# Kernel tuning notes

Measured on AMD Instinct MI355X. Metric: run time of the kernel, lower is better.

The kernel has to match this reference:

```python
import math
import jax, jax.numpy as jnp
import numpy as np

B = 512
E = 512
C = 70722
M_MARGIN = 0.4
H = 0.333
S = 64.0
T_ALPHA = 1.0
EPS = 1e-3


def setup_inputs() -> dict:
    key = jax.random.key(0)
    k1, k2, k3, k4 = jax.random.split(key, 4)
    embbedings = jax.random.normal(k1, (B, E), dtype=jnp.float32)
    embbedings = embbedings / jnp.linalg.norm(embbedings, axis=1, keepdims=True)
    # feature norms typically ~[10, 30] for face models
    norms = 10.0 + 20.0 * jax.random.uniform(k2, (B, 1), dtype=jnp.float32)
    label = jax.random.randint(k3, (B,), 0, C, dtype=jnp.int64)
    kernel = jax.random.normal(k4, (E, C), dtype=jnp.float32)
    batch_mean = jnp.ones((C,), dtype=jnp.float32) * 20.0
    batch_std = jnp.asarray(10.0, dtype=jnp.float32)
    return {"embbedings": embbedings, "norms": norms, "label": label,
            "kernel": kernel, "batch_mean": batch_mean, "batch_std": batch_std}


def reference(embbedings, norms, label, kernel, batch_mean, batch_std):
    # column-wise l2-normalize the class weight matrix [E, C]
    kernel_norm = kernel / jnp.linalg.norm(kernel, axis=0, keepdims=True)
    cosine = jnp.clip(embbedings @ kernel_norm, -1.0 + EPS, 1.0 - EPS)  # [B, C]
    safe_norms = jnp.clip(norms, 1e-3, 100.0)  # [B, 1]

    # ---- running-stat update (torch.no_grad block) ----
    sn = jax.lax.stop_gradient(safe_norms[:, 0])  # [B]
    sums = jnp.zeros((C,), dtype=sn.dtype).at[label].add(sn)
    counts = jnp.zeros((C,), dtype=sn.dtype).at[label].add(1.0)
    group_mean = sums / jnp.maximum(counts, 1.0)  # per-class batch mean of norms
    new_mean = jnp.where(counts > 0,
                         group_mean * T_ALPHA + (1.0 - T_ALPHA) * batch_mean,
                         batch_mean)
    std = jnp.std(sn, ddof=1)  # torch.std is unbiased
    new_std = std * T_ALPHA + (1.0 - T_ALPHA) * batch_std

    # ---- adaptive margin ----
    margin_scaler = (safe_norms - new_mean[label][:, None]) / (new_std + EPS)
    margin_scaler = jnp.clip(margin_scaler * H, -1.0, 1.0)  # [B, 1]

    oh = jax.nn.one_hot(label, C, dtype=cosine.dtype)  # [B, C]
    g_angular = -M_MARGIN * margin_scaler               # [B, 1]
    theta = jnp.arccos(cosine)
    theta_m = jnp.clip(theta + oh * g_angular, EPS, math.pi - EPS)
    g_add = M_MARGIN + M_MARGIN * margin_scaler         # [B, 1]
    out = (jnp.cos(theta_m) - oh * g_add) * S
    return out
```

## Files before the change

kernel.cpp:

```cpp
#include <hip/hip_runtime.h>
#include <hip/hip_bf16.h>
#include <cstdint>
#include <cstddef>
#include <math.h>

#define B_SZ 512
#define E_SZ 512
#define C_SZ 70722
#define PAD_C 70784
#define M_MARGIN 0.4f
#define H_CONST 0.333f
#define S_CONST 64.0f
#define EPS_F 1e-3f
#define PI_F 3.14159265358979323846f

typedef __attribute__((ext_vector_type(8))) short short8;
typedef __attribute__((ext_vector_type(4))) float f32x4;


__device__ __forceinline__ unsigned short f2bf(float x) {
  __hip_bfloat16 h = __float2bfloat16(x);
  unsigned short u;
  __builtin_memcpy(&u, &h, 2);
  return u;
}

__device__ __forceinline__ void gload_lds16(const void* g, void* l) {
  __builtin_amdgcn_global_load_lds(
      (const __attribute__((address_space(1))) unsigned int*)g,
      (__attribute__((address_space(3))) unsigned int*)l, 16, 0, 0);
}

__device__ __forceinline__ int swzb(int rc) {
  return (((rc & 7) ^ ((rc >> 2) & 7)) << 4);
}

__global__ void k_stats(const float* __restrict__ norms, const int* __restrict__ label,
                        float* __restrict__ ga, float* __restrict__ gadd) {
  __shared__ float sn[B_SZ];
  __shared__ int lab[B_SZ];
  __shared__ float redA[8], redB[8];
  __shared__ float sh_std;

  int t = threadIdx.x;
  float v = norms[t];
  v = fminf(fmaxf(v, 1e-3f), 100.0f);
  sn[t] = v;
  lab[t] = label[t];

  float s1 = v, s2 = v * v;
  #pragma unroll
  for (int o = 32; o > 0; o >>= 1) {
    s1 += __shfl_down(s1, o);
    s2 += __shfl_down(s2, o);
  }
  if ((t & 63) == 0) { redA[t >> 6] = s1; redB[t >> 6] = s2; }
  __syncthreads();
  if (t == 0) {
    float a = 0.f, b = 0.f;
    #pragma unroll
    for (int i = 0; i < 8; ++i) { a += redA[i]; b += redB[i]; }
    float mean = a / (float)B_SZ;
    float var = (b - (float)B_SZ * mean * mean) / (float)(B_SZ - 1);
    sh_std = sqrtf(fmaxf(var, 0.f));
  }
  __syncthreads();
  float stdv = sh_std;

  int myl = lab[t];
  float s = 0.f, cnt = 0.f;
  for (int j = 0; j < B_SZ; ++j) {
    bool m = (lab[j] == myl);
    s += m ? sn[j] : 0.f;
    cnt += m ? 1.f : 0.f;
  }
  float gm = s / fmaxf(cnt, 1.f);
  float ms = (v - gm) / (stdv + EPS_F) * H_CONST;
  ms = fminf(fmaxf(ms, -1.f), 1.f);
  ga[t] = -M_MARGIN * ms;
  gadd[t] = M_MARGIN + M_MARGIN * ms;
}

__global__ void k_cvtA(const float* __restrict__ emb, unsigned short* __restrict__ abf) {
  int i = (blockIdx.x * 256 + threadIdx.x) * 4;
  float4 f = *(const float4*)(emb + i);
  unsigned short u0 = f2bf(f.x), u1 = f2bf(f.y), u2 = f2bf(f.z), u3 = f2bf(f.w);
  unsigned long long pk = (unsigned long long)u0 | ((unsigned long long)u1 << 16) |
                          ((unsigned long long)u2 << 32) | ((unsigned long long)u3 << 48);
  *(unsigned long long*)(abf + i) = pk;
}

__global__ void k_colnorm(const float* __restrict__ K, float* __restrict__ inv) {
  __shared__ float part[4][64];
  int cl = threadIdx.x & 63;
  int rq = threadIdx.x >> 6;
  int c = blockIdx.x * 64 + cl;
  float s = 0.f;
  if (c < C_SZ) {
    const float* p = K + (size_t)rq * 128 * C_SZ + c;
    #pragma unroll 8
    for (int r = 0; r < 128; ++r) {
      float x = p[(size_t)r * C_SZ];
      s += x * x;
    }
  }
  part[rq][cl] = s;
  __syncthreads();
  if (threadIdx.x < 64) {
    int c2 = blockIdx.x * 64 + threadIdx.x;
    if (c2 < C_SZ) {
      float tt = part[0][threadIdx.x] + part[1][threadIdx.x] +
                 part[2][threadIdx.x] + part[3][threadIdx.x];
      inv[c2] = rsqrtf(tt);
    } else if (c2 < PAD_C) {
      inv[c2] = 0.f;
    }
  }
}

__launch_bounds__(256)
__global__ void k_gemm(const unsigned short* __restrict__ Abf,
                       const float* __restrict__ Kmat,
                       const float* __restrict__ invn,
                       const int* __restrict__ label,
                       const float* __restrict__ ga,
                       const float* __restrict__ gadd,
                       float* __restrict__ out) {
  __shared__ __align__(16) unsigned short As[128 * 64];
  __shared__ __align__(16) unsigned short Bs[128 * 64];
  __shared__ int lab_s[128];
  __shared__ float ga_s[128], gadd_s[128];

  const int tid = threadIdx.x;
  const int nwg = gridDim.x;
  int bid = blockIdx.x;

  int q = nwg >> 3, r8 = nwg & 7;
  int xcd = bid & 7, lb = bid >> 3;
  int wg = (xcd < r8 ? xcd * (q + 1) : r8 * (q + 1) + (xcd - r8) * q) + lb;

  const int mt = wg & 3;
  const int nt = wg >> 2;
  const int row0 = mt << 7;
  const int col0 = nt << 7;

  if (tid < 128) {
    int gr = row0 + tid;
    lab_s[tid] = label[gr];
    ga_s[tid] = ga[gr];
    gadd_s[tid] = gadd[gr];
  }

  const int wid = tid >> 6, lane = tid & 63;
  const int wr = wid >> 1, wc = wid & 1;

  const int cc = tid & 31;
  const int kq = tid >> 5;

  const bool edge = (col0 + 128 > C_SZ);
  float4 inv4 = *(const float4*)(invn + col0 + cc * 4);

  f32x4 acc[4][4];
  #pragma unroll
  for (int m = 0; m < 4; ++m)
    #pragma unroll
    for (int n = 0; n < 4; ++n)
      acc[m][n] = f32x4{0.f, 0.f, 0.f, 0.f};

  const float* Bg = Kmat + col0;

  for (int kt = 0; kt < 8; ++kt) {
    const int kb = kt * 64;
    if (kt) __syncthreads();

    #pragma unroll
    for (int rr = 0; rr < 4; ++rr) {
      int rowblk = wid * 32 + rr * 8;
      int r = rowblk + (lane >> 3);
      int s = (lane & 7) ^ ((r & 7) ^ ((r >> 2) & 7));
      const unsigned short* g = Abf + (size_t)(row0 + r) * 512 + kb + s * 8;
      gload_lds16(g, (char*)As + rowblk * 128);
    }

    #pragma unroll
    for (int i = 0; i < 4; ++i) {
      int k = (kq + i * 8) * 2;
      const float* g0 = Bg + (size_t)(kb + k) * C_SZ + cc * 4;
      const float* g1 = g0 + C_SZ;
      float x0[4], x1[4];
      if (!edge) {
        float4 f0 = *(const float4*)g0;
        float4 f1 = *(const float4*)g1;
        x0[0] = f0.x; x0[1] = f0.y; x0[2] = f0.z; x0[3] = f0.w;
        x1[0] = f1.x; x1[1] = f1.y; x1[2] = f1.z; x1[3] = f1.w;
      } else {
        #pragma unroll
        for (int j = 0; j < 4; ++j) {
          int gc = col0 + cc * 4 + j;
          x0[j] = (gc < C_SZ) ? g0[j] : 0.f;
          x1[j] = (gc < C_SZ) ? g1[j] : 0.f;
        }
      }
      #pragma unroll
      for (int j = 0; j < 4; ++j) {
        int c = cc * 4 + j;
        float iv = ((const float*)&inv4)[j];
        unsigned int pk = ((unsigned int)f2bf(x1[j] * iv) << 16) | (unsigned int)f2bf(x0[j] * iv);
        int byte = (c * 128 + k * 2) ^ swzb(c);
        *(unsigned int*)((char*)Bs + byte) = pk;
      }
    }

    __syncthreads();

    #pragma unroll
    for (int ks = 0; ks < 2; ++ks) {
      short8 a[4], b[4];
      #pragma unroll
      for (int m = 0; m < 4; ++m) {
        int row = wr * 64 + m * 16 + (lane & 15);
        int off = (row * 128 + ks * 64 + (lane >> 4) * 16) ^ swzb(row);
        a[m] = *(const short8*)((const char*)As + off);
      }
      #pragma unroll
      for (int n = 0; n < 4; ++n) {
        int c = wc * 64 + n * 16 + (lane & 15);
        int off = (c * 128 + ks * 64 + (lane >> 4) * 16) ^ swzb(c);
        b[n] = *(const short8*)((const char*)Bs + off);
      }
      #pragma unroll
      for (int m = 0; m < 4; ++m)
        #pragma unroll
        for (int n = 0; n < 4; ++n)
          acc[m][n] = __builtin_amdgcn_mfma_f32_16x16x32_bf16(a[m], b[n], acc[m][n], 0, 0, 0);
    }
  }

  #pragma unroll
  for (int m = 0; m < 4; ++m) {
    int rl0 = wr * 64 + m * 16 + ((lane >> 4) << 2);
    #pragma unroll
    for (int n = 0; n < 4; ++n) {
      int cl = wc * 64 + n * 16 + (lane & 15);
      int gc = col0 + cl;
      if (gc >= C_SZ) continue;
      #pragma unroll
      for (int r = 0; r < 4; ++r) {
        int rl = rl0 + r;
        float v = acc[m][n][r];
        v = fminf(fmaxf(v, -1.f + EPS_F), 1.f - EPS_F);
        float res = v * S_CONST;
        if (gc == lab_s[rl]) {
          float th = acosf(v) + ga_s[rl];
          th = fminf(fmaxf(th, EPS_F), PI_F - EPS_F);
          res = (cosf(th) - gadd_s[rl]) * S_CONST;
        }
        out[(size_t)(row0 + rl) * C_SZ + gc] = res;
      }
    }
  }
}

extern "C" void kernel_launch(void* const* d_in, const int* in_sizes, int n_in,
                              void* d_out, int out_size, void* d_ws, size_t ws_size,
                              hipStream_t stream) {
  const float* emb   = (const float*)d_in[0];
  const float* norms = (const float*)d_in[1];
  const int*   label = (const int*)d_in[2];
  const float* kmat  = (const float*)d_in[3];
  float* out = (float*)d_out;

  if (ws_size < 812032) return;
  char* ws = (char*)d_ws;
  float* invn = (float*)ws;
  float* ga   = (float*)(ws + 283648);
  float* gadd = (float*)(ws + 285696);
  unsigned short* abf = (unsigned short*)(ws + 287744);

  k_stats<<<1, 512, 0, stream>>>(norms, label, ga, gadd);
  k_cvtA<<<256, 256, 0, stream>>>(emb, abf);
  k_colnorm<<<1106, 256, 0, stream>>>(kmat, invn);
  k_gemm<<<2212, 256, 0, stream>>>(abf, kmat, invn, label, ga, gadd, out);
}
```

Measured before the change: 159.8 us.

## Pre-transpose kernel to bf16 K-major layout and apply column norm in epilogue

A new prep kernel reads the fp32 class-weight matrix once. In that single pass it computes the column sums of squares and writes a transposed bf16 copy (C x 512) to the workspace. The GEMM then loads both operands with direct global-to-LDS 16-byte loads, and applies the inverse column norm in the epilogue instead of scaling and converting B during the main loop. This removes the fp32 B reads and the per-tile convert/scatter work from the GEMM, and folds the separate column-norm pass into the transpose. The cost is an extra ~72MB bf16 write and read, and the fast path needs a large workspace, with a fallback to the old path when the workspace is too small.

```diff
diff --git a/kernel.cpp b/kernel.cpp
--- a/kernel.cpp
+++ b/kernel.cpp
@@ -89,6 +89,187 @@
                           ((unsigned long long)u2 << 32) | ((unsigned long long)u3 << 48);
   *(unsigned long long*)(abf + i) = pk;
 }
+
+__global__ void k_prep(const float* __restrict__ K, float* __restrict__ invn,
+                       unsigned short* __restrict__ BT) {
+  __shared__ float T[64 * 64];
+  __shared__ float part[16][64];
+
+  const int t = threadIdx.x;
+  const int c0 = blockIdx.x * 64;
+  const int cl = t & 15;
+  const int kr = t >> 4;
+  const int cq = t >> 2;
+  const int kq = t & 3;
+  const bool full = (c0 + 64 <= C_SZ);
+
+  float ss0 = 0.f, ss1 = 0.f, ss2 = 0.f, ss3 = 0.f;
+
+  for (int ch = 0; ch < 8; ++ch) {
+    if (ch) __syncthreads();
+    #pragma unroll
+    for (int i = 0; i < 4; ++i) {
+      int klo = kr + i * 16;
+      int kg = ch * 64 + klo;
+      float4 f;
+      if (full) {
+        f = *(const float4*)(K + (size_t)kg * C_SZ + c0 + cl * 4);
+      } else {
+        float* fp = (float*)&f;
+        #pragma unroll
+        for (int j = 0; j < 4; ++j) {
+          int c = c0 + cl * 4 + j;
+          fp[j] = (c < C_SZ) ? K[(size_t)kg * C_SZ + c] : 0.f;
+        }
+      }
+      ss0 += f.x * f.x; ss1 += f.y * f.y; ss2 += f.z * f.z; ss3 += f.w * f.w;
+      int swz = (klo & 7) << 2;
+      *(float4*)&T[klo * 64 + ((cl * 4) ^ swz)] = f;
+    }
+    __syncthreads();
+    #pragma unroll
+    for (int sub = 0; sub < 2; ++sub) {
+      int k8 = sub * 32 + kq * 8;
+      short8 v;
+      #pragma unroll
+      for (int i = 0; i < 8; ++i) {
+        v[i] = (short)f2bf(T[(k8 + i) * 64 + (cq ^ (i << 2))]);
+      }
+      *(short8*)(BT + ((size_t)(c0 + cq) << 9) + ch * 64 + k8) = v;
+    }
+  }
+
+  __syncthreads();
+  part[kr][cl * 4 + 0] = ss0;
+  part[kr][cl * 4 + 1] = ss1;
+  part[kr][cl * 4 + 2] = ss2;
+  part[kr][cl * 4 + 3] = ss3;
+  __syncthreads();
+  if (t < 64) {
+    int c = c0 + t;
+    float s = 0.f;
+    #pragma unroll
+    for (int r = 0; r < 16; ++r) s += part[r][t];
+    invn[c] = (c < C_SZ) ? rsqrtf(s) : 0.f;
+  }
+}
+
+__launch_bounds__(256)
+__global__ void k_gemm_fast(const unsigned short* __restrict__ Abf,
+                            const unsigned short* __restrict__ BT,
+                            const float* __restrict__ invn,
+                            const int* __restrict__ label,
+                            const float* __restrict__ ga,
+                            const float* __restrict__ gadd,
+                            float* __restrict__ out) {
+  __shared__ __align__(16) unsigned short As[128 * 64];
+  __shared__ __align__(16) unsigned short Bs[128 * 64];
+  __shared__ int lab_s[128];
+  __shared__ float ga_s[128], gadd_s[128];
+
+  const int tid = threadIdx.x;
+  const int nwg = gridDim.x;
+  int bid = blockIdx.x;
+
+  int q = nwg >> 3, r8 = nwg & 7;
+  int xcd = bid & 7, lb = bid >> 3;
+  int wg = (xcd < r8 ? xcd * (q + 1) : r8 * (q + 1) + (xcd - r8) * q) + lb;
+
+  const int mt = wg & 3;
+  const int nt = wg >> 2;
+  const int row0 = mt << 7;
+  const int col0 = nt << 7;
+
+  if (tid < 128) {
+    int gr = row0 + tid;
+    lab_s[tid] = label[gr];
+    ga_s[tid] = ga[gr];
+    gadd_s[tid] = gadd[gr];
+  }
+
+  const int wid = tid >> 6, lane = tid & 63;
+  const int wr = wid >> 1, wc = wid & 1;
+
+  f32x4 acc[4][4];
+  #pragma unroll
+  for (int m = 0; m < 4; ++m)
+    #pragma unroll
+    for (int n = 0; n < 4; ++n)
+      acc[m][n] = f32x4{0.f, 0.f, 0.f, 0.f};
+
+  const int rsub = lane >> 3;
+  const int lchunk = lane & 7;
+
+  for (int kt = 0; kt < 8; ++kt) {
+    const int kb = kt * 64;
+    if (kt) __syncthreads();
+
+    #pragma unroll
+    for (int rr = 0; rr < 4; ++rr) {
+      int rowblk = wid * 32 + rr * 8;
+      int r = rowblk + rsub;
+      int s = lchunk ^ ((r & 7) ^ ((r >> 2) & 7));
+      gload_lds16(Abf + (size_t)(row0 + r) * 512 + kb + s * 8,
+                  (char*)As + rowblk * 128);
+      gload_lds16(BT + (size_t)(col0 + r) * 512 + kb + s * 8,
+                  (char*)Bs + rowblk * 128);
+    }
+
+    __syncthreads();
+
+    #pragma unroll
+    for (int ks = 0; ks < 2; ++ks) {
+      short8 a[4], b[4];
+      #pragma unroll
+      for (int m = 0; m < 4; ++m) {
+        int row = wr * 64 + m * 16 + (lane & 15);
+        int off = (row * 128 + ks * 64 + (lane >> 4) * 16) ^ swzb(row);
+        a[m] = *(const short8*)((const char*)As + off);
+      }
+      #pragma unroll
+      for (int n = 0; n < 4; ++n) {
+        int c = wc * 64 + n * 16 + (lane & 15);
+        int off = (c * 128 + ks * 64 + (lane >> 4) * 16) ^ swzb(c);
+        b[n] = *(const short8*)((const char*)Bs + off);
+      }
+      #pragma unroll
+      for (int m = 0; m < 4; ++m)
+        #pragma unroll
+        for (int n = 0; n < 4; ++n)
+          acc[m][n] = __builtin_amdgcn_mfma_f32_16x16x32_bf16(a[m], b[n], acc[m][n], 0, 0, 0);
+    }
+  }
+
+  float invc[4];
+  #pragma unroll
+  for (int n = 0; n < 4; ++n)
+    invc[n] = invn[col0 + wc * 64 + n * 16 + (lane & 15)];
+
+  #pragma unroll
+  for (int m = 0; m < 4; ++m) {
+    int rl0 = wr * 64 + m * 16 + ((lane >> 4) << 2);
+    #pragma unroll
+    for (int n = 0; n < 4; ++n) {
+      int cl = wc * 64 + n * 16 + (lane & 15);
+      int gc = col0 + cl;
+      if (gc >= C_SZ) continue;
+      #pragma unroll
+      for (int r = 0; r < 4; ++r) {
+        int rl = rl0 + r;
+        float v = acc[m][n][r] * invc[n];
+        v = fminf(fmaxf(v, -1.f + EPS_F), 1.f - EPS_F);
+        float res = v * S_CONST;
+        if (gc == lab_s[rl]) {
+          float th = acosf(v) + ga_s[rl];
+          th = fminf(fmaxf(th, EPS_F), PI_F - EPS_F);
+          res = (cosf(th) - gadd_s[rl]) * S_CONST;
+        }
+        out[(size_t)(row0 + rl) * C_SZ + gc] = res;
+      }
+    }
+  }
+}
+
 
 __global__ void k_colnorm(const float* __restrict__ K, float* __restrict__ inv) {
   __shared__ float part[4][64];
@@ -119,13 +300,13 @@
 }
 
 __launch_bounds__(256)
-__global__ void k_gemm(const unsigned short* __restrict__ Abf,
-                       const float* __restrict__ Kmat,
-                       const float* __restrict__ invn,
-                       const int* __restrict__ label,
-                       const float* __restrict__ ga,
-                       const float* __restrict__ gadd,
-                       float* __restrict__ out) {
+__global__ void k_gemm_fb(const unsigned short* __restrict__ Abf,
+                          const float* __restrict__ Kmat,
+                          const float* __restrict__ invn,
+                          const int* __restrict__ label,
+                          const float* __restrict__ ga,
+                          const float* __restrict__ gadd,
+                          float* __restrict__ out) {
   __shared__ __align__(16) unsigned short As[128 * 64];
   __shared__ __align__(16) unsigned short Bs[128 * 64];
   __shared__ int lab_s[128];
@@ -134,11 +315,9 @@
   const int tid = threadIdx.x;
   const int nwg = gridDim.x;
   int bid = blockIdx.x;
-
   int q = nwg >> 3, r8 = nwg & 7;
   int xcd = bid & 7, lb = bid >> 3;
   int wg = (xcd < r8 ? xcd * (q + 1) : r8 * (q + 1) + (xcd - r8) * q) + lb;
-
   const int mt = wg & 3;
   const int nt = wg >> 2;
   const int row0 = mt << 7;
@@ -153,10 +332,8 @@
 
   const int wid = tid >> 6, lane = tid & 63;
   const int wr = wid >> 1, wc = wid & 1;
-
   const int cc = tid & 31;
   const int kq = tid >> 5;
-
   const bool edge = (col0 + 128 > C_SZ);
   float4 inv4 = *(const float4*)(invn + col0 + cc * 4);
 
@@ -178,8 +355,7 @@
       int rowblk = wid * 32 + rr * 8;
       int r = rowblk + (lane >> 3);
       int s = (lane & 7) ^ ((r & 7) ^ ((r >> 2) & 7));
-      const unsigned short* g = Abf + (size_t)(row0 + r) * 512 + kb + s * 8;
-      gload_lds16(g, (char*)As + rowblk * 128);
+      gload_lds16(Abf + (size_t)(row0 + r) * 512 + kb + s * 8, (char*)As + rowblk * 128);
     }
 
     #pragma unroll
@@ -191,8 +367,8 @@
       if (!edge) {
         float4 f0 = *(const float4*)g0;
         float4 f1 = *(const float4*)g1;
-        x0[0] = f0.x; x0[1] = f0.y; x0[2] = f0.z; x0[3] = f0.w;
-        x1[0] = f1.x; x1[1] = f1.y; x1[2] = f1.z; x1[3] = f1.w;
+        x0[0]=f0.x; x0[1]=f0.y; x0[2]=f0.z; x0[3]=f0.w;
+        x1[0]=f1.x; x1[1]=f1.y; x1[2]=f1.z; x1[3]=f1.w;
       } else {
         #pragma unroll
         for (int j = 0; j < 4; ++j) {
@@ -270,15 +446,22 @@
   const float* kmat  = (const float*)d_in[3];
   float* out = (float*)d_out;
 
-  if (ws_size < 812032) return;
+  const size_t NEED_FAST = 73294336;
   char* ws = (char*)d_ws;
   float* invn = (float*)ws;
-  float* ga   = (float*)(ws + 283648);
-  float* gadd = (float*)(ws + 285696);
-  unsigned short* abf = (unsigned short*)(ws + 287744);
+  float* ga   = (float*)(ws + 283136);
+  float* gadd = (float*)(ws + 285184);
+  unsigned short* abf = (unsigned short*)(ws + 287232);
+  unsigned short* bt  = (unsigned short*)(ws + 811520);
 
   k_stats<<<1, 512, 0, stream>>>(norms, label, ga, gadd);
   k_cvtA<<<256, 256, 0, stream>>>(emb, abf);
-  k_colnorm<<<1106, 256, 0, stream>>>(kmat, invn);
-  k_gemm<<<2212, 256, 0, stream>>>(abf, kmat, invn, label, ga, gadd, out);
-}
+
+  if (ws_size >= NEED_FAST) {
+    k_prep<<<1106, 256, 0, stream>>>(kmat, invn, bt);
+    k_gemm_fast<<<2212, 256, 0, stream>>>(abf, bt, invn, label, ga, gadd, out);
+  } else {
+    k_colnorm<<<1106, 256, 0, stream>>>(kmat, invn);
+    k_gemm_fb<<<2212, 256, 0, stream>>>(abf, kmat, invn, label, ga, gadd, out);
+  }
+}
```

Measured after the change: 150.1 us. 6.0% less time.

## Fuse column-norm into full-batch GEMM with double-buffered B staging

Applied to the files above, without the earlier changes.

Drops the separate column-norm kernel and computes each column's sum of squares inside the GEMM while the kernel tile is loaded, applying the inverse norm to the accumulators in the epilogue. Each block now covers all 512 rows for a 64-column slice, so the fp32 kernel matrix is read from global memory once instead of twice for norms and four times for M-tiles. B staging is double-buffered with a register prefetch and a shuffle-based transpose, and the K step is 32. The cost is 512-thread blocks with a 32KB A tile held in LDS, a register-heavy prefetch path, and two barriers per K step.

```diff
diff --git a/kernel.cpp b/kernel.cpp
--- a/kernel.cpp
+++ b/kernel.cpp
@@ -7,7 +7,8 @@
 #define B_SZ 512
 #define E_SZ 512
 #define C_SZ 70722
-#define PAD_C 70784
+#define BN 64
+#define NBLK 1106
 #define M_MARGIN 0.4f
 #define H_CONST 0.333f
 #define S_CONST 64.0f
@@ -29,10 +30,6 @@
   __builtin_amdgcn_global_load_lds(
       (const __attribute__((address_space(1))) unsigned int*)g,
       (__attribute__((address_space(3))) unsigned int*)l, 16, 0, 0);
-}
-
-__device__ __forceinline__ int swzb(int rc) {
-  return (((rc & 7) ^ ((rc >> 2) & 7)) << 4);
 }
 
 __global__ void k_stats(const float* __restrict__ norms, const int* __restrict__ label,
@@ -90,75 +87,52 @@
   *(unsigned long long*)(abf + i) = pk;
 }
 
-__global__ void k_colnorm(const float* __restrict__ K, float* __restrict__ inv) {
-  __shared__ float part[4][64];
-  int cl = threadIdx.x & 63;
-  int rq = threadIdx.x >> 6;
-  int c = blockIdx.x * 64 + cl;
-  float s = 0.f;
-  if (c < C_SZ) {
-    const float* p = K + (size_t)rq * 128 * C_SZ + c;
-    #pragma unroll 8
-    for (int r = 0; r < 128; ++r) {
-      float x = p[(size_t)r * C_SZ];
-      s += x * x;
-    }
-  }
-  part[rq][cl] = s;
-  __syncthreads();
-  if (threadIdx.x < 64) {
-    int c2 = blockIdx.x * 64 + threadIdx.x;
-    if (c2 < C_SZ) {
-      float tt = part[0][threadIdx.x] + part[1][threadIdx.x] +
-                 part[2][threadIdx.x] + part[3][threadIdx.x];
-      inv[c2] = rsqrtf(tt);
-    } else if (c2 < PAD_C) {
-      inv[c2] = 0.f;
-    }
-  }
-}
-
-__launch_bounds__(256)
-__global__ void k_gemm(const unsigned short* __restrict__ Abf,
-                       const float* __restrict__ Kmat,
-                       const float* __restrict__ invn,
-                       const int* __restrict__ label,
-                       const float* __restrict__ ga,
-                       const float* __restrict__ gadd,
-                       float* __restrict__ out) {
-  __shared__ __align__(16) unsigned short As[128 * 64];
-  __shared__ __align__(16) unsigned short Bs[128 * 64];
-  __shared__ int lab_s[128];
-  __shared__ float ga_s[128], gadd_s[128];
+__launch_bounds__(512, 4)
+__global__ void k_gemm_full(const unsigned short* __restrict__ Abf,
+                            const float* __restrict__ Kmat,
+                            const int* __restrict__ label,
+                            const float* __restrict__ ga,
+                            const float* __restrict__ gadd,
+                            float* __restrict__ out) {
+  __shared__ __align__(16) unsigned short As[512 * 32];
+  __shared__ __align__(16) unsigned short Bs[2][BN * 32];
+  __shared__ float red[8][BN];
+  __shared__ float invn_s[BN];
+  __shared__ int lab_s[512];
 
   const int tid = threadIdx.x;
-  const int nwg = gridDim.x;
-  int bid = blockIdx.x;
-
-  int q = nwg >> 3, r8 = nwg & 7;
-  int xcd = bid & 7, lb = bid >> 3;
-  int wg = (xcd < r8 ? xcd * (q + 1) : r8 * (q + 1) + (xcd - r8) * q) + lb;
-
-  const int mt = wg & 3;
-  const int nt = wg >> 2;
-  const int row0 = mt << 7;
-  const int col0 = nt << 7;
-
-  if (tid < 128) {
-    int gr = row0 + tid;
-    lab_s[tid] = label[gr];
-    ga_s[tid] = ga[gr];
-    gadd_s[tid] = gadd[gr];
-  }
-
-  const int wid = tid >> 6, lane = tid & 63;
-  const int wr = wid >> 1, wc = wid & 1;
-
-  const int cc = tid & 31;
-  const int kq = tid >> 5;
-
-  const bool edge = (col0 + 128 > C_SZ);
-  float4 inv4 = *(const float4*)(invn + col0 + cc * 4);
+  const int w = tid >> 6;
+  const int lane = tid & 63;
+  const int q = lane >> 4;
+  const int l15 = lane & 15;
+
+  const int c0 = blockIdx.x * BN;
+  const bool edge = (c0 + BN > C_SZ);
+
+  lab_s[tid] = label[tid];
+
+  const int r_loc = tid >> 4;
+  const int bcol = c0 + (l15 << 2);
+  const int cT = (l15 << 2) + q;
+  const int sigT = l15 & 3;
+  char* const bwr = (char*)&Bs[0][0] + cT * 64 + (((w >> 1) ^ sigT) & 3) * 16 + ((w & 1) << 3);
+
+  const int arow_l = lane >> 2;
+  const int acg = (lane & 3) ^ q;
+  char* const adst = (char*)As + (w * 64) * 64;
+
+  const int sfrag = l15 >> 2;
+  int offA[4], offB[4];
+  #pragma unroll
+  for (int m = 0; m < 4; ++m) {
+    int row = w * 64 + m * 16 + l15;
+    offA[m] = row * 64 + ((q ^ sfrag) & 3) * 16;
+  }
+  #pragma unroll
+  for (int n = 0; n < 4; ++n) {
+    int c = n * 16 + l15;
+    offB[n] = c * 64 + ((q ^ sfrag) & 3) * 16;
+  }
 
   f32x4 acc[4][4];
   #pragma unroll
@@ -167,95 +141,140 @@
     for (int n = 0; n < 4; ++n)
       acc[m][n] = f32x4{0.f, 0.f, 0.f, 0.f};
 
-  const float* Bg = Kmat + col0;
-
-  for (int kt = 0; kt < 8; ++kt) {
-    const int kb = kt * 64;
-    if (kt) __syncthreads();
-
-    #pragma unroll
-    for (int rr = 0; rr < 4; ++rr) {
-      int rowblk = wid * 32 + rr * 8;
-      int r = rowblk + (lane >> 3);
-      int s = (lane & 7) ^ ((r & 7) ^ ((r >> 2) & 7));
-      const unsigned short* g = Abf + (size_t)(row0 + r) * 512 + kb + s * 8;
-      gload_lds16(g, (char*)As + rowblk * 128);
+  float ss0 = 0.f, ss1 = 0.f, ss2 = 0.f, ss3 = 0.f;
+
+#define BLOAD(bv, kb)                                                        \
+  {                                                                          \
+    const float* src = Kmat + (size_t)((kb) + r_loc) * C_SZ + bcol;          \
+    if (!edge) {                                                             \
+      bv = *(const float4*)src;                                              \
+    } else {                                                                 \
+      bv.x = (bcol + 0 < C_SZ) ? src[0] : 0.f;                               \
+      bv.y = (bcol + 1 < C_SZ) ? src[1] : 0.f;                               \
+      bv.z = (bcol + 2 < C_SZ) ? src[2] : 0.f;                               \
+      bv.w = (bcol + 3 < C_SZ) ? src[3] : 0.f;                               \
+    }                                                                        \
+  }
+
+#define BXPOSE_WRITE(bv, buf)                                                \
+  {                                                                          \
+    ss0 += bv.x * bv.x; ss1 += bv.y * bv.y;                                  \
+    ss2 += bv.z * bv.z; ss3 += bv.w * bv.w;                                  \
+    bool h32 = (lane & 32) != 0;                                             \
+    float t2 = h32 ? bv.x : bv.z;                                            \
+    float t3 = h32 ? bv.y : bv.w;                                            \
+    float x2 = __shfl_xor(t2, 32);                                           \
+    float x3 = __shfl_xor(t3, 32);                                           \
+    float u0 = h32 ? x2 : bv.x;                                              \
+    float u1 = h32 ? x3 : bv.y;                                              \
+    float u2 = h32 ? bv.z : x2;                                              \
+    float u3 = h32 ? bv.w : x3;                                              \
+    bool h16 = (lane & 16) != 0;                                             \
+    float s0 = h16 ? u0 : u1;                                                \
+    float s1 = h16 ? u2 : u3;                                                \
+    float z0 = __shfl_xor(s0, 16);                                           \
+    float z1 = __shfl_xor(s1, 16);                                           \
+    float y0 = h16 ? z0 : u0;                                                \
+    float y1 = h16 ? u1 : z0;                                                \
+    float y2 = h16 ? z1 : u2;                                                \
+    float y3 = h16 ? u3 : z1;                                                \
+    unsigned long long pk = (unsigned long long)f2bf(y0) |                   \
+                            ((unsigned long long)f2bf(y1) << 16) |           \
+                            ((unsigned long long)f2bf(y2) << 32) |           \
+                            ((unsigned long long)f2bf(y3) << 48);            \
+    *(unsigned long long*)(bwr + (buf) * 4096) = pk;                         \
+  }
+
+#define ASTAGE(kb)                                                           \
+  {                                                                          \
+    _Pragma("unroll")                                                        \
+    for (int rr = 0; rr < 4; ++rr) {                                         \
+      int r = w * 64 + rr * 16 + arow_l;                                     \
+      gload_lds16(Abf + (size_t)r * 512 + (kb) + acg * 8, adst + rr * 1024); \
+    }                                                                        \
+  }
+
+  ASTAGE(0)
+  {
+    float4 bv;
+    BLOAD(bv, 0)
+    BXPOSE_WRITE(bv, 0)
+  }
+  __syncthreads();
+
+  for (int kt = 0; kt < 16; ++kt) {
+    const int cur = kt & 1;
+
+    float4 bv;
+    if (kt < 15) BLOAD(bv, (kt + 1) * 32)
+
+    short8 a[4], b[4];
+    const char* pB = (const char*)&Bs[0][0] + cur * 4096;
+    #pragma unroll
+    for (int m = 0; m < 4; ++m) a[m] = *(const short8*)((const char*)As + offA[m]);
+    #pragma unroll
+    for (int n = 0; n < 4; ++n) b[n] = *(const short8*)(pB + offB[n]);
+
+    #pragma unroll
+    for (int m = 0; m < 4; ++m)
+      #pragma unroll
+      for (int n = 0; n < 4; ++n)
+        acc[m][n] = __builtin_amdgcn_mfma_f32_16x16x32_bf16(a[m], b[n], acc[m][n], 0, 0, 0);
+
+    __syncthreads();
+
+    if (kt < 15) {
+      ASTAGE((kt + 1) * 32)
+      BXPOSE_WRITE(bv, cur ^ 1)
     }
-
-    #pragma unroll
-    for (int i = 0; i < 4; ++i) {
-      int k = (kq + i * 8) * 2;
-      const float* g0 = Bg + (size_t)(kb + k) * C_SZ + cc * 4;
-      const float* g1 = g0 + C_SZ;
-      float x0[4], x1[4];
-      if (!edge) {
-        float4 f0 = *(const float4*)g0;
-        float4 f1 = *(const float4*)g1;
-        x0[0] = f0.x; x0[1] = f0.y; x0[2] = f0.z; x0[3] = f0.w;
-        x1[0] = f1.x; x1[1] = f1.y; x1[2] = f1.z; x1[3] = f1.w;
-      } else {
-        #pragma unroll
-        for (int j = 0; j < 4; ++j) {
-          int gc = col0 + cc * 4 + j;
-          x0[j] = (gc < C_SZ) ? g0[j] : 0.f;
-          x1[j] = (gc < C_SZ) ? g1[j] : 0.f;
-        }
-      }
-      #pragma unroll
-      for (int j = 0; j < 4; ++j) {
-        int c = cc * 4 + j;
-        float iv = ((const float*)&inv4)[j];
-        unsigned int pk = ((unsigned int)f2bf(x1[j] * iv) << 16) | (unsigned int)f2bf(x0[j] * iv);
-        int byte = (c * 128 + k * 2) ^ swzb(c);
-        *(unsigned int*)((char*)Bs + byte) = pk;
-      }
-    }
-
     __syncthreads();
-
-    #pragma unroll
-    for (int ks = 0; ks < 2; ++ks) {
-      short8 a[4], b[4];
-      #pragma unroll
-      for (int m = 0; m < 4; ++m) {
-        int row = wr * 64 + m * 16 + (lane & 15);
-        int off = (row * 128 + ks * 64 + (lane >> 4) * 16) ^ swzb(row);
-        a[m] = *(const short8*)((const char*)As + off);
-      }
-      #pragma unroll
-      for (int n = 0; n < 4; ++n) {
-        int c = wc * 64 + n * 16 + (lane & 15);
-        int off = (c * 128 + ks * 64 + (lane >> 4) * 16) ^ swzb(c);
-        b[n] = *(const short8*)((const char*)Bs + off);
-      }
-      #pragma unroll
-      for (int m = 0; m < 4; ++m)
-        #pragma unroll
-        for (int n = 0; n < 4; ++n)
-          acc[m][n] = __builtin_amdgcn_mfma_f32_16x16x32_bf16(a[m], b[n], acc[m][n], 0, 0, 0);
-    }
-  }
+  }
+#undef BLOAD
+#undef BXPOSE_WRITE
+#undef ASTAGE
+
+  ss0 += __shfl_xor(ss0, 16); ss0 += __shfl_xor(ss0, 32);
+  ss1 += __shfl_xor(ss1, 16); ss1 += __shfl_xor(ss1, 32);
+  ss2 += __shfl_xor(ss2, 16); ss2 += __shfl_xor(ss2, 32);
+  ss3 += __shfl_xor(ss3, 16); ss3 += __shfl_xor(ss3, 32);
+  if (lane < 16) {
+    red[w][l15 * 4 + 0] = ss0;
+    red[w][l15 * 4 + 1] = ss1;
+    red[w][l15 * 4 + 2] = ss2;
+    red[w][l15 * 4 + 3] = ss3;
+  }
+  __syncthreads();
+  if (tid < BN) {
+    float s = 0.f;
+    #pragma unroll
+    for (int r = 0; r < 8; ++r) s += red[r][tid];
+    invn_s[tid] = (s > 0.f) ? rsqrtf(s) : 0.f;
+  }
+  __syncthreads();
+
+  float invc[4];
+  #pragma unroll
+  for (int n = 0; n < 4; ++n) invc[n] = invn_s[n * 16 + l15];
 
   #pragma unroll
   for (int m = 0; m < 4; ++m) {
-    int rl0 = wr * 64 + m * 16 + ((lane >> 4) << 2);
+    int grow0 = w * 64 + m * 16 + q * 4;
     #pragma unroll
     for (int n = 0; n < 4; ++n) {
-      int cl = wc * 64 + n * 16 + (lane & 15);
-      int gc = col0 + cl;
+      int gc = c0 + n * 16 + l15;
       if (gc >= C_SZ) continue;
       #pragma unroll
       for (int r = 0; r < 4; ++r) {
-        int rl = rl0 + r;
-        float v = acc[m][n][r];
+        int grow = grow0 + r;
+        float v = acc[m][n][r] * invc[n];
         v = fminf(fmaxf(v, -1.f + EPS_F), 1.f - EPS_F);
         float res = v * S_CONST;
-        if (gc == lab_s[rl]) {
-          float th = acosf(v) + ga_s[rl];
+        if (gc == lab_s[grow]) {
+          float th = acosf(v) + ga[grow];
           th = fminf(fmaxf(th, EPS_F), PI_F - EPS_F);
-          res = (cosf(th) - gadd_s[rl]) * S_CONST;
+          res = (cosf(th) - gadd[grow]) * S_CONST;
         }
-        out[(size_t)(row0 + rl) * C_SZ + gc] = res;
+        out[(size_t)grow * C_SZ + gc] = res;
       }
     }
   }
@@ -270,15 +289,12 @@
   const float* kmat  = (const float*)d_in[3];
   float* out = (float*)d_out;
 
-  if (ws_size < 812032) return;
   char* ws = (char*)d_ws;
-  float* invn = (float*)ws;
-  float* ga   = (float*)(ws + 283648);
-  float* gadd = (float*)(ws + 285696);
-  unsigned short* abf = (unsigned short*)(ws + 287744);
+  float* ga   = (float*)ws;
+  float* gadd = (float*)(ws + 2048);
+  unsigned short* abf = (unsigned short*)(ws + 4096);
 
   k_stats<<<1, 512, 0, stream>>>(norms, label, ga, gadd);
   k_cvtA<<<256, 256, 0, stream>>>(emb, abf);
-  k_colnorm<<<1106, 256, 0, stream>>>(kmat, invn);
-  k_gemm<<<2212, 256, 0, stream>>>(abf, kmat, invn, label, ga, gadd, out);
-}
+  k_gemm_full<<<NBLK, 512, 0, stream>>>(abf, kmat, label, ga, gadd, out);
+}
```

New measurement: 150.4 us. 1.06x faster.
